# Kernel optimization log

Measured on AMD Instinct MI355X. Metric: run time of the kernel, lower is better.

The kernel has to match this reference:

```python
import jax, jax.numpy as jnp
import numpy as np

N, E, B = 524288, 4194304, 16384
F_IN, FP, TV, GOUT = 14, 1024, 256, 32
EPS = 1e-5
SLOPE = 0.2  # PyG GATConv default negative_slope


def setup_inputs() -> dict:
    key = jax.random.key(0)
    ks = iter(jax.random.split(key, 64))
    def nrm(shape, scale=1.0):
        return jax.random.normal(next(ks), shape, dtype=jnp.float32) * scale
    def uni(shape, lo, hi):
        return jax.random.uniform(next(ks), shape, dtype=jnp.float32, minval=lo, maxval=hi)
    def bn(d):  # [gamma, beta, running_mean, running_var]
        return jnp.stack([uni((d,), 0.5, 1.5), nrm((d,), 0.1), nrm((d,), 0.1), uni((d,), 0.5, 1.5)])
    return {
        'x': nrm((N, F_IN)),
        'edge_index': jax.random.randint(next(ks), (2, E), 0, N, dtype=jnp.int32),
        'batch': jnp.sort(jax.random.randint(next(ks), (N,), 0, B, dtype=jnp.int32)),
        'fingerprint': nrm((B, FP)),
        'transformer_features': nrm((B, TV)),
        'W1': nrm((F_IN, F_IN), 0.3), 'a_src1': nrm((F_IN,), 0.3), 'a_dst1': nrm((F_IN,), 0.3), 'b1': nrm((F_IN,), 0.1),
        'W2': nrm((F_IN, GOUT), 0.3), 'a_src2': nrm((GOUT,), 0.3), 'a_dst2': nrm((GOUT,), 0.3), 'b2': nrm((GOUT,), 0.1),
        'fc1_w': nrm((FP, 400), 0.04), 'fc1_b': nrm((400,), 0.1), 'bn1': bn(400),
        'fc2_w': nrm((400, 200), 0.07), 'fc2_b': nrm((200,), 0.1), 'bn2': bn(200),
        'fc3_w': nrm((TV, 400), 0.08), 'fc3_b': nrm((400,), 0.1), 'bn3': bn(400),
        'fc4_w': nrm((400, 200), 0.07), 'fc4_b': nrm((200,), 0.1), 'bn4': bn(200),
        'fcc1_w': nrm((GOUT + 400, 100), 0.07), 'fcc1_b': nrm((100,), 0.1), 'bnc': bn(100),
        'fcc2_w': nrm((100, 1), 0.1), 'fcc2_b': nrm((1,), 0.1),
    }


def _bn(h, p):  # eval-mode BatchNorm1d with packed params [4, d]
    return (h - p[2]) * jax.lax.rsqrt(p[3] + EPS) * p[0] + p[1]


def _gat(x, W, a_s, a_d, b, src, dst, n):
    # PyG GATConv, heads=1: messages flow src -> dst, softmax over incoming edges per dst
    h = x @ W                                   # [n, C]
    e = jax.nn.leaky_relu((h @ a_s)[src] + (h @ a_d)[dst], SLOPE)  # [E_tot]
    m = jax.lax.stop_gradient(jax.ops.segment_max(e, dst, num_segments=n))
    w = jnp.exp(e - m[dst])
    denom = jax.ops.segment_sum(w, dst, num_segments=n)
    alpha = w / denom[dst]
    out = jax.ops.segment_sum(alpha[:, None] * h[src], dst, num_segments=n)
    return out + b


def reference(x, edge_index, batch, fingerprint, transformer_features,
              W1, a_src1, a_dst1, b1, W2, a_src2, a_dst2, b2,
              fc1_w, fc1_b, bn1, fc2_w, fc2_b, bn2,
              fc3_w, fc3_b, bn3, fc4_w, fc4_b, bn4,
              fcc1_w, fcc1_b, bnc, fcc2_w, fcc2_b):
    n = x.shape[0]
    loop = jnp.arange(n, dtype=edge_index.dtype)  # add_self_loops
    src = jnp.concatenate([edge_index[0], loop])
    dst = jnp.concatenate([edge_index[1], loop])
    g = jax.nn.relu(_gat(x, W1, a_src1, a_dst1, b1, src, dst, n))
    g = jax.nn.relu(_gat(g, W2, a_src2, a_dst2, b2, src, dst, n))
    pool = jax.ops.segment_sum(g, batch, num_segments=B)  # global_add_pool -> [B, GOUT]
    fp = jax.nn.relu(_bn(fingerprint @ fc1_w + fc1_b, bn1))
    fp = jax.nn.relu(_bn(fp @ fc2_w + fc2_b, bn2))
    tv = jax.nn.relu(_bn(transformer_features @ fc3_w + fc3_b, bn3))
    tv = jax.nn.relu(_bn(tv @ fc4_w + fc4_b, bn4))
    comb = jnp.concatenate([pool, fp, tv], axis=1)  # [B, 32+200+200]
    comb = jax.nn.relu(_bn(comb @ fcc1_w + fcc1_b, bnc))
    return comb @ fcc2_w + fcc2_b  # [B, 1]
```

## Files before the change

kernel.cpp:

```cpp
#include <hip/hip_runtime.h>

typedef unsigned short u16;
typedef unsigned int u32;
typedef __attribute__((ext_vector_type(8))) short bf16x8;
typedef __attribute__((ext_vector_type(4))) float f32x4;

#define N_NODES 524288
#define N_EDGES 4194304
#define N_GRAPH 16384
#define P_BLOCKS 1024
#define BKTS 512
#define DPB 1024
#define CAP 8960

__device__ __forceinline__ float bf2f(u16 u){ u32 x=((u32)u)<<16; float f; __builtin_memcpy(&f,&x,4); return f; }
__device__ __forceinline__ float lo2f(u32 u){ u32 x=u<<16; float f; __builtin_memcpy(&f,&x,4); return f; }
__device__ __forceinline__ float hi2f(u32 u){ u32 x=u&0xffff0000u; float f; __builtin_memcpy(&f,&x,4); return f; }
__device__ __forceinline__ u16 f2bf(float f){ u32 x; __builtin_memcpy(&x,&f,4); return (u16)((x + 0x7fffu + ((x>>16)&1u))>>16); }
__device__ __forceinline__ float lrelu(float e){ return e>0.f? e : 0.2f*e; }
__device__ __forceinline__ float gload(const void* p, int i, int is32){
    return is32 ? ((const float*)p)[i] : bf2f(((const u16*)p)[i]);
}
__device__ __forceinline__ u32 fmax_key(float f){ u32 u; __builtin_memcpy(&u,&f,4); return (u>>31)? ~u : (u|0x80000000u); }
__device__ __forceinline__ float key_fmax(u32 k){ u32 u = (k>>31)? (k^0x80000000u) : ~k; float f; __builtin_memcpy(&f,&u,4); return f; }

__device__ __forceinline__ void edge_acc(uint4 q0, uint4 q1, float adv, float M,
        float* acc, float& den){
    float as_; __builtin_memcpy(&as_, &q1.w, 4);
    float w = __expf(lrelu(as_ + adv) - M); den += w;
    u32 u[7] = {q0.x,q0.y,q0.z,q0.w,q1.x,q1.y,q1.z};
    #pragma unroll
    for (int f=0;f<14;f++){ u32 uu=u[f>>1]; acc[f] += w*((f&1)? hi2f(uu):lo2f(uu)); }
}

__global__ __launch_bounds__(256) void k_detect(const u32* __restrict__ x, int* __restrict__ flag){
    __shared__ int cnt;
    if (threadIdx.x==0) cnt = 0;
    __syncthreads();
    int c = 0;
    for (int i = threadIdx.x; i < 1024; i += 256){
        u32 e = (x[i] >> 7) & 0xFF;
        if (e >= 110 && e <= 140) c++;
    }
    atomicAdd(&cnt, c);
    __syncthreads();
    if (threadIdx.x==0) *flag = (cnt < 512) ? 1 : 0;
}

__global__ __launch_bounds__(64) void k_prep(const void* __restrict__ W2, const void* __restrict__ asw,
        const void* __restrict__ adw, float* __restrict__ prep, const int* __restrict__ flag){
    int is32 = *flag;
    int t = threadIdx.x;
    if (t < 28){
        int j = t % 14, which = t / 14;
        const void* av = which ? adw : asw;
        float s = 0.f;
        #pragma unroll
        for (int k=0;k<32;k++) s += gload(W2, j*32+k, is32) * gload(av, k, is32);
        prep[which*14 + j] = s;
    }
}

__global__ __launch_bounds__(256) void k_cast(const void* __restrict__ in, u16* __restrict__ out,
        int n8, const int* __restrict__ flag){
    int is32 = *flag;
    int idx = blockIdx.x*256 + threadIdx.x;
    if (idx >= n8) return;
    if (is32){
        const float4* ip = (const float4*)in + idx*2;
        float4 a0 = ip[0], a1 = ip[1];
        u32 w0 = (u32)f2bf(a0.x) | ((u32)f2bf(a0.y)<<16);
        u32 w1 = (u32)f2bf(a0.z) | ((u32)f2bf(a0.w)<<16);
        u32 w2 = (u32)f2bf(a1.x) | ((u32)f2bf(a1.y)<<16);
        u32 w3 = (u32)f2bf(a1.z) | ((u32)f2bf(a1.w)<<16);
        ((uint4*)out)[idx] = make_uint4(w0,w1,w2,w3);
    } else {
        ((uint4*)out)[idx] = ((const uint4*)in)[idx];
    }
}

__global__ __launch_bounds__(256) void k_p1(const int* __restrict__ dst, u32* __restrict__ tbl_bm){
    __shared__ u32 lh[BKTS];
    int t = threadIdx.x, blk = blockIdx.x;
    lh[t] = 0; lh[t+256] = 0;
    __syncthreads();
    int base = blk*4096;
    #pragma unroll
    for (int k=0;k<16;k++){
        int d = __builtin_nontemporal_load(dst + base + k*256 + t) & (N_NODES-1);
        atomicAdd(&lh[d>>10], 1);
    }
    __syncthreads();
    tbl_bm[blk*BKTS + t]       = lh[t];
    tbl_bm[blk*BKTS + t + 256] = lh[t+256];
}

__global__ __launch_bounds__(256) void k_ttbl(const u32* __restrict__ bm, u32* __restrict__ km){
    __shared__ u32 tile[32][33];
    int bx = blockIdx.x, by = blockIdx.y;
    int tx = threadIdx.x & 31, ty = threadIdx.x >> 5;
    #pragma unroll
    for (int r=0;r<32;r+=8)
        tile[ty+r][tx] = bm[(bx*32 + ty + r)*BKTS + by*32 + tx];
    __syncthreads();
    #pragma unroll
    for (int r=0;r<32;r+=8)
        km[(by*32 + ty + r)*P_BLOCKS + bx*32 + tx] = tile[tx][ty+r];
}

__global__ __launch_bounds__(256) void k_scan1(int* __restrict__ data, int* __restrict__ bsums){
    __shared__ int sh[256];
    int b = blockIdx.x, t = threadIdx.x;
    int base = b*1024 + t*4;
    int4 v = *(const int4*)(data + base);
    int s = v.x+v.y+v.z+v.w;
    sh[t] = s; __syncthreads();
    for (int off=1; off<256; off<<=1){
        int xv = (t>=off)? sh[t-off] : 0; __syncthreads();
        sh[t] += xv; __syncthreads();
    }
    int excl = sh[t] - s;
    if (t==255) bsums[b] = sh[255];
    int4 o; o.x = excl; o.y = excl+v.x; o.z = o.y+v.y; o.w = o.z+v.z;
    *(int4*)(data + base) = o;
}

__global__ __launch_bounds__(256) void k_scan2(int* __restrict__ bsums){
    __shared__ int sh[256];
    int t = threadIdx.x;
    int v0 = bsums[2*t], v1 = bsums[2*t+1];
    int s = v0+v1; sh[t] = s; __syncthreads();
    for (int off=1; off<256; off<<=1){
        int xv = (t>=off)? sh[t-off] : 0; __syncthreads();
        sh[t] += xv; __syncthreads();
    }
    int excl = sh[t] - s;
    bsums[2*t] = excl; bsums[2*t+1] = excl + v0;
}

__global__ __launch_bounds__(256) void k_scan3(int* __restrict__ scan, const int* __restrict__ bsums, int N_, int E_){
    int i = blockIdx.x*256 + threadIdx.x;
    if (i < N_) scan[i] += bsums[i>>10];
    if (i == 0) scan[N_] = E_;
}

__global__ __launch_bounds__(256) void k_p2(const int* __restrict__ src, const int* __restrict__ dst,
        const u32* __restrict__ km, u32* __restrict__ btab){
    __shared__ u32 lh[BKTS], lofs[BKTS], gofs[BKTS];
    __shared__ u32 stage[4096], tgt[4096];
    __shared__ u32 red[256];
    int t = threadIdx.x, blk = blockIdx.x;
    lh[t] = 0; lh[t+256] = 0;
    __syncthreads();
    u32 pr[16], rk[16]; u16 bk[16];
    int base = blk*4096;
    #pragma unroll
    for (int k=0;k<16;k++){
        int e = base + k*256 + t;
        int d = __builtin_nontemporal_load(dst+e) & (N_NODES-1);
        int s = __builtin_nontemporal_load(src+e) & (N_NODES-1);
        u32 b = (u32)d >> 10;
        bk[k] = (u16)b;
        pr[k] = (u32)(d & 1023) | ((u32)s << 10);
        rk[k] = atomicAdd(&lh[b], 1);
    }
    gofs[t]       = km[(size_t)t*P_BLOCKS + blk];
    gofs[t+256]   = km[(size_t)(t+256)*P_BLOCKS + blk];
    __syncthreads();
    u32 v0 = lh[2*t], v1 = lh[2*t+1];
    u32 s2 = v0+v1; red[t] = s2; __syncthreads();
    for (int off=1; off<256; off<<=1){
        u32 xv = (t>=off)? red[t-off] : 0; __syncthreads();
        red[t] += xv; __syncthreads();
    }
    u32 excl = red[t] - s2;
    lofs[2*t] = excl; lofs[2*t+1] = excl + v0;
    __syncthreads();
    #pragma unroll
    for (int k=0;k<16;k++){
        u32 p = lofs[bk[k]] + rk[k];
        stage[p] = pr[k];
        tgt[p]   = gofs[bk[k]] + rk[k];
    }
    __syncthreads();
    #pragma unroll
    for (int k=0;k<16;k++){
        int j = k*256 + t;
        btab[tgt[j]] = stage[j];
    }
}

__global__ __launch_bounds__(256) void k_p3(const u32* __restrict__ km, const u32* __restrict__ btab,
        int* __restrict__ rowptr, int* __restrict__ ssrc){
    __shared__ u32 fh[DPB], fo[DPB];
    __shared__ u32 red[256];
    __shared__ int sst[CAP];
    int t = threadIdx.x, b = blockIdx.x;
    u32 basep = km[(size_t)b*P_BLOCKS];
    u32 endp  = km[(size_t)(b+1)*P_BLOCKS];
    int cnt = (int)(endp - basep);
    #pragma unroll
    for (int i=t;i<DPB;i+=256) fh[i] = 0;
    __syncthreads();
    for (int j=t; j<cnt; j+=256){
        u32 p = btab[basep + j];
        atomicAdd(&fh[p & 1023], 1);
    }
    __syncthreads();
    u32 v0=fh[4*t], v1=fh[4*t+1], v2=fh[4*t+2], v3=fh[4*t+3];
    u32 s4 = v0+v1+v2+v3; red[t] = s4; __syncthreads();
    for (int off=1; off<256; off<<=1){
        u32 xv = (t>=off)? red[t-off] : 0; __syncthreads();
        red[t] += xv; __syncthreads();
    }
    u32 excl = red[t] - s4;
    fo[4*t]=excl; fo[4*t+1]=excl+v0; fo[4*t+2]=excl+v0+v1; fo[4*t+3]=excl+v0+v1+v2;
    __syncthreads();
    #pragma unroll
    for (int i=t;i<DPB;i+=256) rowptr[b*DPB + i] = (int)(basep + fo[i]);
    if (b == BKTS-1 && t == 0) rowptr[N_NODES] = (int)endp;
    __syncthreads();
    for (int j=t; j<cnt; j+=256){
        u32 p = btab[basep + j];
        u32 pos = atomicAdd(&fo[p & 1023], 1);
        if (pos < (u32)CAP) sst[pos] = (int)(p >> 10);
    }
    __syncthreads();
    for (int j=t; j<cnt; j+=256) ssrc[basep + j] = sst[j];
}

__global__ __launch_bounds__(256) void k_linear1(const void* __restrict__ x,
        const void* __restrict__ W1, const void* __restrict__ asw, const void* __restrict__ adw,
        u16* __restrict__ h1, float* __restrict__ ad1, u32* __restrict__ gkey,
        const int* __restrict__ flag){
    int is32 = *flag;
    __shared__ float Wf[196], av[14], dv[14];
    __shared__ float red[256];
    int t = threadIdx.x;
    if (t < 196) Wf[t] = gload(W1, t, is32);
    else if (t < 210) av[t-196] = gload(asw, t-196, is32);
    else if (t < 224) dv[t-210] = gload(adw, t-210, is32);
    __syncthreads();
    int i = blockIdx.x*256 + t;
    float xv[14];
    if (is32){
        const float* xr = (const float*)x + (size_t)i*14;
        #pragma unroll
        for (int k=0;k<14;k++) xv[k] = xr[k];
    } else {
        const u32* xr = (const u32*)((const u16*)x + (size_t)i*14);
        #pragma unroll
        for (int p=0;p<7;p++){ u32 u = xr[p]; xv[2*p]=lo2f(u); xv[2*p+1]=hi2f(u); }
    }
    float h[14];
    #pragma unroll
    for (int j=0;j<14;j++){ float s=0.f;
        #pragma unroll
        for (int k=0;k<14;k++) s += xv[k]*Wf[k*14+j];
        h[j]=s; }
    float a=0.f, d=0.f;
    #pragma unroll
    for (int j=0;j<14;j++){ a += h[j]*av[j]; d += h[j]*dv[j]; }
    ad1[i]=d;
    u32 ou[8];
    #pragma unroll
    for (int p=0;p<7;p++) ou[p] = (u32)f2bf(h[2*p]) | ((u32)f2bf(h[2*p+1])<<16);
    __builtin_memcpy(&ou[7], &a, 4);
    uint4* hp = (uint4*)(h1 + (size_t)i*16);
    hp[0] = make_uint4(ou[0],ou[1],ou[2],ou[3]);
    hp[1] = make_uint4(ou[4],ou[5],ou[6],ou[7]);
    red[t] = a; __syncthreads();
    for (int o=128;o;o>>=1){ if (t<o) red[t]=fmaxf(red[t],red[t+o]); __syncthreads(); }
    if (t==0) atomicMax(gkey, fmax_key(red[0]));
}

__global__ __launch_bounds__(256) void k_gather1(const int* __restrict__ rowptr, const int* __restrict__ ssrc,
        const u16* __restrict__ h1, const float* __restrict__ ad1, const u32* __restrict__ gkey1,
        const void* __restrict__ b1, const float* __restrict__ prep,
        u16* __restrict__ g1, float* __restrict__ ad2, u32* __restrict__ gkey2,
        const int* __restrict__ flag){
    int is32 = *flag;
    __shared__ float b1s[14], vas[14], vds[14];
    __shared__ float red[256];
    int t = threadIdx.x;
    if (t < 14) b1s[t] = gload(b1, t, is32);
    else if (t < 28) vas[t-14] = prep[t-14];
    else if (t < 42) vds[t-28] = prep[t-28+14];
    __syncthreads();
    int i = blockIdx.x*256 + t;
    float adv = ad1[i];
    float M = lrelu(key_fmax(*gkey1) + adv);
    int beg = rowptr[i], end = rowptr[i+1];
    float acc[14] = {0,0,0,0,0,0,0,0,0,0,0,0,0,0};
    float den = 0.f;
    {
        const uint4* hp = (const uint4*)(h1 + (size_t)i*16);
        edge_acc(hp[0], hp[1], adv, M, acc, den);
    }
    int j = beg;
    for (; j+4 <= end; j += 4){
        int s4[4];
        #pragma unroll
        for (int k=0;k<4;k++) s4[k] = __builtin_nontemporal_load(ssrc + j + k);
        uint4 r0[4], r1[4];
        #pragma unroll
        for (int k=0;k<4;k++){
            const uint4* hp = (const uint4*)(h1 + (size_t)s4[k]*16);
            r0[k] = hp[0]; r1[k] = hp[1];
        }
        #pragma unroll
        for (int k=0;k<4;k++) edge_acc(r0[k], r1[k], adv, M, acc, den);
    }
    for (; j<end; j++){
        int s = __builtin_nontemporal_load(ssrc + j);
        const uint4* hp = (const uint4*)(h1 + (size_t)s*16);
        edge_acc(hp[0], hp[1], adv, M, acc, den);
    }
    float inv = 1.0f/den;
    float v[14];
    #pragma unroll
    for (int f=0;f<14;f++) v[f] = fmaxf(acc[f]*inv + b1s[f], 0.f);
    float a2=0.f, d2=0.f;
    #pragma unroll
    for (int f=0;f<14;f++){ a2 += v[f]*vas[f]; d2 += v[f]*vds[f]; }
    ad2[i] = d2;
    u32 ou[8];
    #pragma unroll
    for (int p=0;p<7;p++) ou[p] = (u32)f2bf(v[2*p]) | ((u32)f2bf(v[2*p+1])<<16);
    __builtin_memcpy(&ou[7], &a2, 4);
    uint4* gp = (uint4*)(g1 + (size_t)i*16);
    gp[0]=make_uint4(ou[0],ou[1],ou[2],ou[3]);
    gp[1]=make_uint4(ou[4],ou[5],ou[6],ou[7]);
    red[t] = a2; __syncthreads();
    for (int o=128;o;o>>=1){ if (t<o) red[t]=fmaxf(red[t],red[t+o]); __syncthreads(); }
    if (t==0) atomicMax(gkey2, fmax_key(red[0]));
}

__global__ __launch_bounds__(256) void k_gather2(const int* __restrict__ rowptr, const int* __restrict__ ssrc,
        const u16* __restrict__ g1, const float* __restrict__ ad2, const u32* __restrict__ gkey2,
        const void* __restrict__ W2, const void* __restrict__ b2, u16* __restrict__ g2,
        const int* __restrict__ flag){
    int is32 = *flag;
    __shared__ float W2s[448], b2s[32];
    int t = threadIdx.x;
    for (int idx=t; idx<448; idx+=256) W2s[idx] = gload(W2, idx, is32);
    if (t < 32) b2s[t] = gload(b2, t, is32);
    __syncthreads();
    int i = blockIdx.x*256 + t;
    float adv = ad2[i];
    float M = lrelu(key_fmax(*gkey2) + adv);
    int beg = rowptr[i], end = rowptr[i+1];
    float acc[14] = {0,0,0,0,0,0,0,0,0,0,0,0,0,0};
    float den = 0.f;
    {
        const uint4* hp = (const uint4*)(g1 + (size_t)i*16);
        edge_acc(hp[0], hp[1], adv, M, acc, den);
    }
    int j = beg;
    for (; j+4 <= end; j += 4){
        int s4[4];
        #pragma unroll
        for (int k=0;k<4;k++) s4[k] = __builtin_nontemporal_load(ssrc + j + k);
        uint4 r0[4], r1[4];
        #pragma unroll
        for (int k=0;k<4;k++){
            const uint4* hp = (const uint4*)(g1 + (size_t)s4[k]*16);
            r0[k] = hp[0]; r1[k] = hp[1];
        }
        #pragma unroll
        for (int k=0;k<4;k++) edge_acc(r0[k], r1[k], adv, M, acc, den);
    }
    for (; j<end; j++){
        int s = __builtin_nontemporal_load(ssrc + j);
        const uint4* hp = (const uint4*)(g1 + (size_t)s*16);
        edge_acc(hp[0], hp[1], adv, M, acc, den);
    }
    float inv = 1.0f/den;
    float an[14];
    #pragma unroll
    for (int f=0;f<14;f++) an[f] = acc[f]*inv;
    uint4* orow = (uint4*)(g2 + (size_t)i*32);
    #pragma unroll
    for (int g=0; g<4; g++){
        u32 ou[4];
        #pragma unroll
        for (int p=0;p<4;p++){
            int j0 = g*8 + 2*p;
            float va_ = b2s[j0], vb_ = b2s[j0+1];
            #pragma unroll
            for (int k=0;k<14;k++){ va_ += an[k]*W2s[k*32+j0]; vb_ += an[k]*W2s[k*32+j0+1]; }
            va_ = fmaxf(va_, 0.f); vb_ = fmaxf(vb_, 0.f);
            ou[p] = (u32)f2bf(va_) | ((u32)f2bf(vb_)<<16);
        }
        orow[g] = make_uint4(ou[0],ou[1],ou[2],ou[3]);
    }
}

__device__ __forceinline__ int lbound(const int* __restrict__ a, int n, int v){
    int lo=0, hi=n;
    while (lo < hi){ int m = (lo+hi)>>1; if (a[m] < v) lo = m+1; else hi = m; }
    return lo;
}

__global__ __launch_bounds__(64) void k_pool(const u16* __restrict__ g2, const int* __restrict__ batch,
        u16* __restrict__ comb, int N_){
    int b = blockIdx.x;
    int t = threadIdx.x, f = t & 31, half = t >> 5;
    int lo = lbound(batch, N_, b);
    int hi = lbound(batch, N_, b+1);
    float acc = 0.f;
    for (int i = lo + half; i < hi; i += 2) acc += bf2f(g2[(size_t)i*32 + f]);
    acc += __shfl_xor(acc, 32);
    if (t < 32) comb[(size_t)b*432 + f] = f2bf(acc);
}

__global__ __launch_bounds__(256) void k_transpose(const void* __restrict__ W, u16* __restrict__ Wt,
        int K, int Kp, int Nc, const int* __restrict__ flag){
    int is32 = *flag;
    int idx = blockIdx.x*256 + threadIdx.x;
    if (idx >= Nc*Kp) return;
    int n = idx / Kp, k = idx - n*Kp;
    Wt[idx] = (k < K) ? f2bf(gload(W, k*Nc + n, is32)) : (u16)0;
}

__global__ __launch_bounds__(256) void k_gemm(const void* __restrict__ A, const u16* __restrict__ Wt,
        const void* __restrict__ bias, const void* __restrict__ bnp, void* __restrict__ out,
        int K, int Kp, int Nc, int ostride, int ooff, int do_relu,
        int out32, const int* __restrict__ flag){
    int is32 = *flag;
    __shared__ u16 As[128][40];
    __shared__ u16 Bs[128][40];
    int t = threadIdx.x;
    int lane = t & 63, wave = t >> 6;
    int bm = blockIdx.x * 128;
    int bn = blockIdx.y * 128;
    int mt = (wave & 1) * 64, nt = (wave >> 1) * 64;
    int quad = lane >> 4, fr = lane & 15;

    f32x4 zero = {0.f, 0.f, 0.f, 0.f};
    f32x4 acc[4][4];
    #pragma unroll
    for (int i=0;i<4;i++)
        #pragma unroll
        for (int j=0;j<4;j++) acc[i][j] = zero;

    int srow0 = t >> 2;
    int scol = (t & 3) * 8;

    for (int k0 = 0; k0 < Kp; k0 += 32){
        #pragma unroll
        for (int h2_=0; h2_<2; h2_++){
            int row = srow0 + h2_*64;
            int gk = k0 + scol;
            uint4 av = make_uint4(0,0,0,0);
            if (gk + 8 <= K) av = *(const uint4*)((const u16*)A + (size_t)(bm+row)*K + gk);
            *(uint4*)(&As[row][scol]) = av;
            uint4 bv = make_uint4(0,0,0,0);
            if (bn + row < Nc) bv = *(const uint4*)(Wt + (size_t)(bn+row)*Kp + gk);
            *(uint4*)(&Bs[row][scol]) = bv;
        }
        __syncthreads();
        bf16x8 af[4], bfr[4];
        #pragma unroll
        for (int i=0;i<4;i++) af[i] = *(const bf16x8*)(&As[mt + i*16 + fr][quad*8]);
        #pragma unroll
        for (int j=0;j<4;j++) bfr[j] = *(const bf16x8*)(&Bs[nt + j*16 + fr][quad*8]);
        #pragma unroll
        for (int i=0;i<4;i++)
            #pragma unroll
            for (int j=0;j<4;j++)
                acc[i][j] = __builtin_amdgcn_mfma_f32_16x16x32_bf16(af[i], bfr[j], acc[i][j], 0, 0, 0);
        __syncthreads();
    }

    #pragma unroll
    for (int j=0;j<4;j++){
        int gn = bn + nt + j*16 + fr;
        if (gn >= Nc) continue;
        float bb = gload(bias, gn, is32);
        float scale = 1.f, shift = bb;
        if (bnp){
            float gm_ = gload(bnp, gn, is32), bt = gload(bnp, Nc+gn, is32);
            float mn = gload(bnp, 2*Nc+gn, is32), vr = gload(bnp, 3*Nc+gn, is32);
            scale = gm_ * rsqrtf(vr + 1e-5f);
            shift = (bb - mn)*scale + bt;
        }
        #pragma unroll
        for (int i=0;i<4;i++){
            #pragma unroll
            for (int r=0;r<4;r++){
                int gm = bm + mt + i*16 + quad*4 + r;
                float v = acc[i][j][r]*scale + shift;
                if (do_relu) v = fmaxf(v, 0.f);
                size_t oidx = (size_t)gm*ostride + ooff + gn;
                if (out32) ((float*)out)[oidx] = v;
                else       ((u16*)out)[oidx] = f2bf(v);
            }
        }
    }
}

__global__ __launch_bounds__(256) void k_fcc2(const float* __restrict__ c1, const void* __restrict__ w,
        const void* __restrict__ b, float* __restrict__ outp, const int* __restrict__ flag){
    int is32 = *flag;
    __shared__ float wf[100];
    int t = threadIdx.x;
    if (t < 100) wf[t] = gload(w, t, is32);
    __syncthreads();
    int i = blockIdx.x*256 + t;
    const float* r = c1 + (size_t)i*100;
    float s = 0.f;
    #pragma unroll 4
    for (int k=0;k<100;k++) s += r[k]*wf[k];
    outp[i] = s + gload(b, 0, is32);
}

extern "C" void kernel_launch(void* const* d_in, const int* in_sizes, int n_in,
                              void* d_out, int out_size, void* d_ws, size_t ws_size,
                              hipStream_t stream){
    const int N = N_NODES, E = N_EDGES;
    const void* x    = d_in[0];
    const int* ei   = (const int*)d_in[1];
    const int* srcA = ei;
    const int* dstA = ei + E;
    const int* batch= (const int*)d_in[2];
    const void* fing = d_in[3];
    const void* tv   = d_in[4];
    const void* W1   = d_in[5];
    const void* as1w = d_in[6];
    const void* ad1w = d_in[7];
    const void* b1   = d_in[8];
    const void* W2   = d_in[9];
    const void* as2w = d_in[10];
    const void* ad2w = d_in[11];
    const void* b2   = d_in[12];
    const void* fc1w = d_in[13]; const void* fc1b = d_in[14]; const void* bn1 = d_in[15];
    const void* fc2w = d_in[16]; const void* fc2b = d_in[17]; const void* bn2 = d_in[18];
    const void* fc3w = d_in[19]; const void* fc3b = d_in[20]; const void* bn3 = d_in[21];
    const void* fc4w = d_in[22]; const void* fc4b = d_in[23]; const void* bn4 = d_in[24];
    const void* fccw = d_in[25]; const void* fccb = d_in[26]; const void* bnc = d_in[27];
    const void* fcc2w= d_in[28]; const void* fcc2b= d_in[29];

    char* ws = (char*)d_ws;
    size_t off = 0;
    auto alloc = [&](size_t bytes)->char*{ char* p = ws + off; off = (off + bytes + 255) & ~(size_t)255; return p; };
    int*  flagp  = (int*)alloc(256);
    u32*  gkey1  = (u32*)flagp + 1;
    u32*  gkey2  = (u32*)flagp + 2;
    float* prep  = (float*)((char*)flagp + 16);
    int*  rowptr = (int*)alloc((size_t)(N+1)*4);
    int*  bsums  = (int*)alloc(513*4);
    u32*  tbl_bm = (u32*)alloc((size_t)BKTS*P_BLOCKS*4);
    u32*  tbl_km = (u32*)alloc(((size_t)BKTS*P_BLOCKS+1)*4);
    int*  ssrc   = (int*)alloc((size_t)E*4);
    u16*  h1     = (u16*)alloc((size_t)N*16*2);
    u16*  g1     = (u16*)alloc((size_t)N*16*2);
    float* ad1_  = (float*)alloc((size_t)N*4);
    float* ad2_  = (float*)alloc((size_t)N*4);
    char* scr32  = alloc((size_t)N*32*2);
    float* c1    = (float*)alloc((size_t)N_GRAPH*100*4);
    u16*  Wt1    = (u16*)alloc((size_t)400*1024*2);
    u16*  Wt2    = (u16*)alloc((size_t)200*416*2);
    u16*  Wt3    = (u16*)alloc((size_t)400*256*2);
    u16*  Wt4    = (u16*)alloc((size_t)200*416*2);
    u16*  Wtc    = (u16*)alloc((size_t)100*448*2);
    u16*  tv_bf  = (u16*)alloc((size_t)N_GRAPH*256*2);
    u32*  btab   = (u32*)scr32;
    u16*  g2     = (u16*)scr32;
    u16*  fp1    = (u16*)scr32;
    u16*  tv1    = (u16*)scr32 + (size_t)N_GRAPH*400;
    u16*  comb   = (u16*)ssrc;
    u16*  fing_bf= h1;

    (void)hipMemsetAsync(flagp, 0, 256, stream);

    k_detect <<<1, 256, 0, stream>>>((const u32*)x, flagp);
    k_prep   <<<1, 64, 0, stream>>>(W2, as2w, ad2w, prep, flagp);
    k_cast   <<<(N_GRAPH*256/8+255)/256, 256, 0, stream>>>(tv, tv_bf, N_GRAPH*256/8, flagp);

    k_p1   <<<P_BLOCKS, 256, 0, stream>>>(dstA, tbl_bm);
    k_ttbl <<<dim3(32,16), 256, 0, stream>>>(tbl_bm, tbl_km);
    k_scan1<<<512,  256, 0, stream>>>((int*)tbl_km, bsums);
    k_scan2<<<1,    256, 0, stream>>>(bsums);
    k_scan3<<<(BKTS*P_BLOCKS)/256, 256, 0, stream>>>((int*)tbl_km, bsums, BKTS*P_BLOCKS, E);
    k_p2   <<<P_BLOCKS, 256, 0, stream>>>(srcA, dstA, tbl_km, btab);
    k_p3   <<<BKTS, 256, 0, stream>>>(tbl_km, btab, rowptr, ssrc);

    k_linear1<<<N/256, 256, 0, stream>>>(x, W1, as1w, ad1w, h1, ad1_, gkey1, flagp);
    k_gather1<<<N/256, 256, 0, stream>>>(rowptr, ssrc, h1, ad1_, gkey1, b1, prep, g1, ad2_, gkey2, flagp);
    k_gather2<<<N/256, 256, 0, stream>>>(rowptr, ssrc, g1, ad2_, gkey2, W2, b2, g2, flagp);
    k_cast   <<<(N_GRAPH*1024/8+255)/256, 256, 0, stream>>>(fing, fing_bf, N_GRAPH*1024/8, flagp);
    k_pool   <<<N_GRAPH, 64, 0, stream>>>(g2, batch, comb, N);

    k_transpose<<<(400*1024+255)/256, 256, 0, stream>>>(fc1w, Wt1, 1024, 1024, 400, flagp);
    k_transpose<<<(200*416 +255)/256, 256, 0, stream>>>(fc2w, Wt2,  400,  416, 200, flagp);
    k_transpose<<<(400*256 +255)/256, 256, 0, stream>>>(fc3w, Wt3,  256,  256, 400, flagp);
    k_transpose<<<(200*416 +255)/256, 256, 0, stream>>>(fc4w, Wt4,  400,  416, 200, flagp);
    k_transpose<<<(100*448 +255)/256, 256, 0, stream>>>(fccw, Wtc,  432,  448, 100, flagp);

    k_gemm<<<dim3(128,4), 256, 0, stream>>>(fing_bf, Wt1, fc1b, bn1, fp1, 1024, 1024, 400, 400,   0, 1, 0, flagp);
    k_gemm<<<dim3(128,2), 256, 0, stream>>>(fp1,  Wt2, fc2b, bn2, comb, 400,  416, 200, 432,  32, 1, 0, flagp);
    k_gemm<<<dim3(128,4), 256, 0, stream>>>(tv_bf, Wt3, fc3b, bn3, tv1, 256,  256, 400, 400,   0, 1, 0, flagp);
    k_gemm<<<dim3(128,2), 256, 0, stream>>>(tv1,  Wt4, fc4b, bn4, comb, 400,  416, 200, 432, 232, 1, 0, flagp);
    k_gemm<<<dim3(128,1), 256, 0, stream>>>(comb, Wtc, fccb, bnc, c1,   432,  448, 100, 100,   0, 1, 1, flagp);

    k_fcc2<<<N_GRAPH/256, 256, 0, stream>>>(c1, fcc2w, fcc2b, (float*)d_out, flagp);
}
```

Baseline: 727.4 us.

## Split each node's edge gather across two lanes and merge detect with prep

The two GAT gather kernels now give each destination node to a pair of threads. Each thread walks alternate incoming edges, the partial sums are combined with a lane shuffle, and the output row writes are split between the pair. The aim is more memory-level parallelism and less load imbalance from varying degree, at the cost of twice the threads and a shuffle reduction. Separately, the k_prep launch is folded into k_detect, removing one tiny kernel launch.

```diff
diff --git a/kernel.cpp b/kernel.cpp
--- a/kernel.cpp
+++ b/kernel.cpp
@@ -33,24 +33,23 @@
     for (int f=0;f<14;f++){ u32 uu=u[f>>1]; acc[f] += w*((f&1)? hi2f(uu):lo2f(uu)); }
 }
 
-__global__ __launch_bounds__(256) void k_detect(const u32* __restrict__ x, int* __restrict__ flag){
-    __shared__ int cnt;
-    if (threadIdx.x==0) cnt = 0;
+__global__ __launch_bounds__(256) void k_detect(const u32* __restrict__ x, int* __restrict__ flag,
+        const void* __restrict__ W2, const void* __restrict__ asw, const void* __restrict__ adw,
+        float* __restrict__ prep){
+    __shared__ int cnt, s32;
+    int t = threadIdx.x;
+    if (t==0) cnt = 0;
     __syncthreads();
     int c = 0;
-    for (int i = threadIdx.x; i < 1024; i += 256){
+    for (int i = t; i < 1024; i += 256){
         u32 e = (x[i] >> 7) & 0xFF;
         if (e >= 110 && e <= 140) c++;
     }
     atomicAdd(&cnt, c);
     __syncthreads();
-    if (threadIdx.x==0) *flag = (cnt < 512) ? 1 : 0;
-}
-
-__global__ __launch_bounds__(64) void k_prep(const void* __restrict__ W2, const void* __restrict__ asw,
-        const void* __restrict__ adw, float* __restrict__ prep, const int* __restrict__ flag){
-    int is32 = *flag;
-    int t = threadIdx.x;
+    if (t==0){ int f = (cnt < 512) ? 1 : 0; *flag = f; s32 = f; }
+    __syncthreads();
+    int is32 = s32;
     if (t < 28){
         int j = t % 14, which = t / 14;
         const void* av = which ? adw : asw;
@@ -274,6 +273,39 @@
     if (t==0) atomicMax(gkey, fmax_key(red[0]));
 }
 
+__device__ __forceinline__ void walk_edges(const int* __restrict__ ssrc, const u16* __restrict__ hsrc,
+        int beg, int end, int sub, float adv, float M, float* acc, float& den){
+    int jj = beg + sub;
+    int c = end - jj; c = (c > 0) ? ((c + 1) >> 1) : 0;
+    while (c >= 4){
+        int s4[4];
+        #pragma unroll
+        for (int k=0;k<4;k++) s4[k] = __builtin_nontemporal_load(ssrc + jj + 2*k);
+        uint4 r0[4], r1[4];
+        #pragma unroll
+        for (int k=0;k<4;k++){
+            const uint4* hp = (const uint4*)(hsrc + (size_t)s4[k]*16);
+            r0[k] = hp[0]; r1[k] = hp[1];
+        }
+        #pragma unroll
+        for (int k=0;k<4;k++) edge_acc(r0[k], r1[k], adv, M, acc, den);
+        jj += 8; c -= 4;
+    }
+    if (c > 0){
+        int s3[3];
+        #pragma unroll
+        for (int k=0;k<3;k++) s3[k] = (k<c) ? __builtin_nontemporal_load(ssrc + jj + 2*k) : 0;
+        uint4 r0[3], r1[3];
+        #pragma unroll
+        for (int k=0;k<3;k++){
+            const uint4* hp = (const uint4*)(hsrc + (size_t)s3[k]*16);
+            r0[k] = hp[0]; r1[k] = hp[1];
+        }
+        #pragma unroll
+        for (int k=0;k<3;k++) if (k<c) edge_acc(r0[k], r1[k], adv, M, acc, den);
+    }
+}
+
 __global__ __launch_bounds__(256) void k_gather1(const int* __restrict__ rowptr, const int* __restrict__ ssrc,
         const u16* __restrict__ h1, const float* __restrict__ ad1, const u32* __restrict__ gkey1,
         const void* __restrict__ b1, const float* __restrict__ prep,
@@ -287,35 +319,21 @@
     else if (t < 28) vas[t-14] = prep[t-14];
     else if (t < 42) vds[t-28] = prep[t-28+14];
     __syncthreads();
-    int i = blockIdx.x*256 + t;
+    int i = blockIdx.x*128 + (t>>1);
+    int sub = t & 1;
     float adv = ad1[i];
     float M = lrelu(key_fmax(*gkey1) + adv);
     int beg = rowptr[i], end = rowptr[i+1];
     float acc[14] = {0,0,0,0,0,0,0,0,0,0,0,0,0,0};
     float den = 0.f;
-    {
+    if (sub == 0){
         const uint4* hp = (const uint4*)(h1 + (size_t)i*16);
         edge_acc(hp[0], hp[1], adv, M, acc, den);
     }
-    int j = beg;
-    for (; j+4 <= end; j += 4){
-        int s4[4];
-        #pragma unroll
-        for (int k=0;k<4;k++) s4[k] = __builtin_nontemporal_load(ssrc + j + k);
-        uint4 r0[4], r1[4];
-        #pragma unroll
-        for (int k=0;k<4;k++){
-            const uint4* hp = (const uint4*)(h1 + (size_t)s4[k]*16);
-            r0[k] = hp[0]; r1[k] = hp[1];
-        }
-        #pragma unroll
-        for (int k=0;k<4;k++) edge_acc(r0[k], r1[k], adv, M, acc, den);
-    }
-    for (; j<end; j++){
-        int s = __builtin_nontemporal_load(ssrc + j);
-        const uint4* hp = (const uint4*)(h1 + (size_t)s*16);
-        edge_acc(hp[0], hp[1], adv, M, acc, den);
-    }
+    walk_edges(ssrc, h1, beg, end, sub, adv, M, acc, den);
+    #pragma unroll
+    for (int f=0;f<14;f++) acc[f] += __shfl_xor(acc[f], 1);
+    den += __shfl_xor(den, 1);
     float inv = 1.0f/den;
     float v[14];
     #pragma unroll
@@ -323,14 +341,21 @@
     float a2=0.f, d2=0.f;
     #pragma unroll
     for (int f=0;f<14;f++){ a2 += v[f]*vas[f]; d2 += v[f]*vds[f]; }
-    ad2[i] = d2;
-    u32 ou[8];
-    #pragma unroll
-    for (int p=0;p<7;p++) ou[p] = (u32)f2bf(v[2*p]) | ((u32)f2bf(v[2*p+1])<<16);
-    __builtin_memcpy(&ou[7], &a2, 4);
+    if (sub == 0) ad2[i] = d2;
     uint4* gp = (uint4*)(g1 + (size_t)i*16);
-    gp[0]=make_uint4(ou[0],ou[1],ou[2],ou[3]);
-    gp[1]=make_uint4(ou[4],ou[5],ou[6],ou[7]);
+    if (sub == 0){
+        u32 o0 = (u32)f2bf(v[0]) | ((u32)f2bf(v[1])<<16);
+        u32 o1 = (u32)f2bf(v[2]) | ((u32)f2bf(v[3])<<16);
+        u32 o2 = (u32)f2bf(v[4]) | ((u32)f2bf(v[5])<<16);
+        u32 o3 = (u32)f2bf(v[6]) | ((u32)f2bf(v[7])<<16);
+        gp[0] = make_uint4(o0,o1,o2,o3);
+    } else {
+        u32 o4 = (u32)f2bf(v[8])  | ((u32)f2bf(v[9])<<16);
+        u32 o5 = (u32)f2bf(v[10]) | ((u32)f2bf(v[11])<<16);
+        u32 o6 = (u32)f2bf(v[12]) | ((u32)f2bf(v[13])<<16);
+        u32 o7; __builtin_memcpy(&o7, &a2, 4);
+        gp[1] = make_uint4(o4,o5,o6,o7);
+    }
     red[t] = a2; __syncthreads();
     for (int o=128;o;o>>=1){ if (t<o) red[t]=fmaxf(red[t],red[t+o]); __syncthreads(); }
     if (t==0) atomicMax(gkey2, fmax_key(red[0]));
@@ -346,42 +371,29 @@
     for (int idx=t; idx<448; idx+=256) W2s[idx] = gload(W2, idx, is32);
     if (t < 32) b2s[t] = gload(b2, t, is32);
     __syncthreads();
-    int i = blockIdx.x*256 + t;
+    int i = blockIdx.x*128 + (t>>1);
+    int sub = t & 1;
     float adv = ad2[i];
     float M = lrelu(key_fmax(*gkey2) + adv);
     int beg = rowptr[i], end = rowptr[i+1];
     float acc[14] = {0,0,0,0,0,0,0,0,0,0,0,0,0,0};
     float den = 0.f;
-    {
+    if (sub == 0){
         const uint4* hp = (const uint4*)(g1 + (size_t)i*16);
         edge_acc(hp[0], hp[1], adv, M, acc, den);
     }
-    int j = beg;
-    for (; j+4 <= end; j += 4){
-        int s4[4];
-        #pragma unroll
-        for (int k=0;k<4;k++) s4[k] = __builtin_nontemporal_load(ssrc + j + k);
-        uint4 r0[4], r1[4];
-        #pragma unroll
-        for (int k=0;k<4;k++){
-            const uint4* hp = (const uint4*)(g1 + (size_t)s4[k]*16);
-            r0[k] = hp[0]; r1[k] = hp[1];
-        }
-        #pragma unroll
-        for (int k=0;k<4;k++) edge_acc(r0[k], r1[k], adv, M, acc, den);
-    }
-    for (; j<end; j++){
-        int s = __builtin_nontemporal_load(ssrc + j);
-        const uint4* hp = (const uint4*)(g1 + (size_t)s*16);
-        edge_acc(hp[0], hp[1], adv, M, acc, den);
-    }
+    walk_edges(ssrc, g1, beg, end, sub, adv, M, acc, den);
+    #pragma unroll
+    for (int f=0;f<14;f++) acc[f] += __shfl_xor(acc[f], 1);
+    den += __shfl_xor(den, 1);
     float inv = 1.0f/den;
     float an[14];
     #pragma unroll
     for (int f=0;f<14;f++) an[f] = acc[f]*inv;
     uint4* orow = (uint4*)(g2 + (size_t)i*32);
     #pragma unroll
-    for (int g=0; g<4; g++){
+    for (int gg=0; gg<2; gg++){
+        int g = gg*2 + sub;
         u32 ou[4];
         #pragma unroll
         for (int p=0;p<4;p++){
@@ -574,8 +586,7 @@
 
     (void)hipMemsetAsync(flagp, 0, 256, stream);
 
-    k_detect <<<1, 256, 0, stream>>>((const u32*)x, flagp);
-    k_prep   <<<1, 64, 0, stream>>>(W2, as2w, ad2w, prep, flagp);
+    k_detect <<<1, 256, 0, stream>>>((const u32*)x, flagp, W2, as2w, ad2w, prep);
     k_cast   <<<(N_GRAPH*256/8+255)/256, 256, 0, stream>>>(tv, tv_bf, N_GRAPH*256/8, flagp);
 
     k_p1   <<<P_BLOCKS, 256, 0, stream>>>(dstA, tbl_bm);
@@ -587,8 +598,8 @@
     k_p3   <<<BKTS, 256, 0, stream>>>(tbl_km, btab, rowptr, ssrc);
 
     k_linear1<<<N/256, 256, 0, stream>>>(x, W1, as1w, ad1w, h1, ad1_, gkey1, flagp);
-    k_gather1<<<N/256, 256, 0, stream>>>(rowptr, ssrc, h1, ad1_, gkey1, b1, prep, g1, ad2_, gkey2, flagp);
-    k_gather2<<<N/256, 256, 0, stream>>>(rowptr, ssrc, g1, ad2_, gkey2, W2, b2, g2, flagp);
+    k_gather1<<<N/128, 256, 0, stream>>>(rowptr, ssrc, h1, ad1_, gkey1, b1, prep, g1, ad2_, gkey2, flagp);
+    k_gather2<<<N/128, 256, 0, stream>>>(rowptr, ssrc, g1, ad2_, gkey2, W2, b2, g2, flagp);
     k_cast   <<<(N_GRAPH*1024/8+255)/256, 256, 0, stream>>>(fing, fing_bf, N_GRAPH*1024/8, flagp);
     k_pool   <<<N_GRAPH, 64, 0, stream>>>(g2, batch, comb, N);
 
```

Result: slower. 853.5 us (+17.3%).
